# Performance work log

Hardware: AMD Instinct MI355X
Metric: run time of the kernel (lower is better)

Reference implementation:

```python
import jax, jax.numpy as jnp
import numpy as np

B, Hn, Wn, C, NH, WS, SR = 4, 64, 64, 256, 8, 3, 8
HD = C // NH
N = Hn * Wn
L = WS * WS
PH, PW = Hn // SR, Wn // SR
P = PH * PW
T = 4096  # cpb table length
NEG = -1e30

def _l2norm(x, axis=-1):
    return x / jnp.maximum(jnp.linalg.norm(x, axis=axis, keepdims=True), 1e-12)

def _unfold(x, ws):
    # x: (B, C, H, W) -> (B, C, ws*ws, H*W), torch F.unfold channel ordering (C major)
    p = ws // 2
    b, c, h, w = x.shape
    xp = jnp.pad(x, ((0, 0), (0, 0), (p, p), (p, p)))
    pats = jnp.stack([xp[:, :, i:i + h, j:j + w] for i in range(ws) for j in range(ws)], axis=2)
    return pats.reshape(b, c, ws * ws, h * w)

def setup_inputs():
    key = jax.random.key(0)
    ks = jax.random.split(key, 16)
    def w(k, shape, s=0.02):
        return jax.random.normal(k, shape, jnp.float32) * s
    # buffers derived from the window geometry (get_seqlen_and_mask)
    ones = np.ones((Hn, Wn), np.float32)
    pad = WS // 2
    op = np.pad(ones, pad)
    pats = np.stack([op[i:i + Hn, j:j + Wn] for i in range(WS) for j in range(WS)], -1).reshape(N, L)
    padding_mask = jnp.asarray(pats == 0)
    seq_length_scale = jnp.asarray(np.log(pats.sum(-1, keepdims=True) + P).astype(np.float32))
    temperature = jnp.log(jnp.expm1(jnp.ones((NH, 1, 1), jnp.float32) / 0.24))
    return dict(
        x=jax.random.normal(ks[0], (B, N, C), jnp.float32),
        relative_pos_index=jax.random.randint(ks[1], (N, P), 0, T),
        relative_coords_table=jax.random.uniform(ks[2], (T, 2), jnp.float32, -1.0, 1.0),
        q_w=w(ks[3], (C, C)), q_b=jnp.zeros((C,), jnp.float32),
        kv_w=w(ks[4], (2 * C, C)), kv_b=jnp.zeros((2 * C,), jnp.float32),
        temperature=temperature,
        query_embedding=w(ks[5], (NH, 1, HD)),
        proj_w=w(ks[6], (C, C)), proj_b=jnp.zeros((C,), jnp.float32),
        sr_w=w(ks[7], (C, C)), sr_b=jnp.zeros((C,), jnp.float32),
        norm_g=jnp.ones((C,), jnp.float32), norm_b=jnp.zeros((C,), jnp.float32),
        cpb1_w=w(ks[8], (512, 2)), cpb1_b=jnp.zeros((512,), jnp.float32),
        cpb2_w=w(ks[9], (NH, 512)), cpb2_b=jnp.zeros((NH,), jnp.float32),
        rpb_local=w(ks[10], (NH, L), 0.0004),
        learnable_tokens=w(ks[11], (NH, HD, L)),
        learnable_bias=jnp.zeros((NH, 1, L), jnp.float32),
        seq_length_scale=seq_length_scale,
        padding_mask=padding_mask,
        H=Hn, W=Wn,
    )

def _forward(x, q_w, q_b, kv_w, kv_b, temperature, query_embedding, proj_w, proj_b,
             sr_w, sr_b, norm_g, norm_b, cpb1_w, cpb1_b, cpb2_w, cpb2_b, rpb_local,
             learnable_tokens, learnable_bias, seq_length_scale, relative_coords_table,
             relative_pos_index, padding_mask, H, W):
    b, n, c = x.shape
    # normalized queries, scaled by learnable temperature and log-seqlen
    q = (x @ q_w.T + q_b).reshape(b, n, NH, HD).transpose(0, 2, 1, 3)  # (B,h,N,d)
    q_norm = _l2norm(q)
    q_scaled = (q_norm + query_embedding[None]) * jax.nn.softplus(temperature)[None] * seq_length_scale
    # --- local branch: sliding-window QK with RPB ---
    kv = x @ kv_w.T + kv_b  # (B,N,2C)
    k_loc = _l2norm((kv[..., :c]).reshape(b, n, NH, HD)).reshape(b, n, c)
    kv_img = jnp.concatenate([k_loc, kv[..., c:]], -1).transpose(0, 2, 1).reshape(b, 2 * c, H, W)
    pats = _unfold(kv_img, WS).reshape(b, 2 * NH, HD, L, n).transpose(0, 1, 4, 2, 3)  # (B,2h,N,d,L)
    k_loc, v_loc = pats[:, :NH], pats[:, NH:]
    attn_local = jnp.einsum('bhnd,bhndl->bhnl', q_scaled, k_loc) + rpb_local[None, :, None, :]
    attn_local = jnp.where(padding_mask[None, None], NEG, attn_local)
    # --- pooled branch ---
    x_img = x.transpose(0, 2, 1).reshape(b, c, H, W)
    x_sr = jax.nn.gelu(jnp.einsum('bchw,oc->bohw', x_img, sr_w) + sr_b[None, :, None, None], approximate=False)
    x_pool = x_sr.reshape(b, c, PH, SR, PW, SR).mean((3, 5)).reshape(b, c, P).transpose(0, 2, 1)  # (B,P,C)
    mu = x_pool.mean(-1, keepdims=True)
    var = x_pool.var(-1, keepdims=True)
    x_pool = (x_pool - mu) / jnp.sqrt(var + 1e-5) * norm_g + norm_b
    kv_pool = (x_pool @ kv_w.T + kv_b).reshape(b, P, 2 * NH, HD).transpose(0, 2, 1, 3)
    k_pool, v_pool = kv_pool[:, :NH], kv_pool[:, NH:]  # (B,h,P,d)
    cpb = jax.nn.relu(relative_coords_table @ cpb1_w.T + cpb1_b) @ cpb2_w.T + cpb2_b  # (T,h)
    pool_bias = cpb.T[:, relative_pos_index.reshape(-1)].reshape(NH, n, P)
    attn_pool = jnp.einsum('bhnd,bhpd->bhnp', q_scaled, _l2norm(k_pool)) + pool_bias[None]
    # --- joint softmax over local + pooled keys ---
    attn = jax.nn.softmax(jnp.concatenate([attn_local, attn_pool], -1), axis=-1)
    attn_local, attn_pool = attn[..., :L], attn[..., L:]
    a = jnp.einsum('bhnd,hdl->bhnl', q_norm, learnable_tokens) + learnable_bias[None] + attn_local
    x_local = jnp.einsum('bhnl,bhndl->bhnd', a, v_loc)
    x_pool_out = jnp.einsum('bhnp,bhpd->bhnd', attn_pool, v_pool)
    out = (x_local + x_pool_out).transpose(0, 2, 1, 3).reshape(b, n, c)
    return out @ proj_w.T + proj_b

def reference(x, relative_pos_index, relative_coords_table, q_w, q_b, kv_w, kv_b, temperature,
              query_embedding, proj_w, proj_b, sr_w, sr_b, norm_g, norm_b, cpb1_w, cpb1_b,
              cpb2_w, cpb2_b, rpb_local, learnable_tokens, learnable_bias, seq_length_scale,
              padding_mask, H, W):
    return _forward(x, q_w, q_b, kv_w, kv_b, temperature, query_embedding, proj_w, proj_b,
                    sr_w, sr_b, norm_g, norm_b, cpb1_w, cpb1_b, cpb2_w, cpb2_b, rpb_local,
                    learnable_tokens, learnable_bias, seq_length_scale, relative_coords_table,
                    relative_pos_index, padding_mask, H, W)
```

## Files before the change

### kernel.cpp

```cpp
#include <hip/hip_runtime.h>
#include <hip/hip_bf16.h>

typedef unsigned short u16;
typedef unsigned int u32;

#define B_ 4
#define N_ 4096
#define C_ 256
#define NH_ 8
#define HD_ 32
#define L_ 9
#define P_ 64
#define T_ 4096
#define NEG_ (-1e30f)

typedef __attribute__((ext_vector_type(8))) short bf16x8;
typedef __attribute__((ext_vector_type(4))) float f32x4;

__device__ __forceinline__ float b2f(u16 u) {
    union { u32 i; float f; } v; v.i = ((u32)u) << 16; return v.f;
}
__device__ __forceinline__ u16 f2b(float f) {
    u32 x = __float_as_uint(f);
    u32 r = (x + 0x7fffu + ((x >> 16) & 1u)) >> 16;
    return (u16)r;
}
__device__ __forceinline__ short f2bs(float f) { return (short)f2b(f); }

__global__ __launch_bounds__(256) void prep_k(
    const float* __restrict__ x, const float* __restrict__ q_w, const float* __restrict__ kv_w,
    const float* __restrict__ sr_w, const float* __restrict__ proj_w,
    u16* __restrict__ xb, u16* __restrict__ wfused, u16* __restrict__ pwb,
    const float* __restrict__ table, const float* __restrict__ w1, const float* __restrict__ b1,
    const float* __restrict__ w2, const float* __restrict__ b2, float* __restrict__ cpb)
{
    __shared__ float w1s[512][2];
    __shared__ float b1s[512];
    __shared__ float w2s[8][512];
    int bid = blockIdx.x, tid = threadIdx.x;
    if (bid < 4096) {
        int i = bid * 256 + tid;
        float4 v = reinterpret_cast<const float4*>(x)[i];
        ushort4 o; o.x = f2b(v.x); o.y = f2b(v.y); o.z = f2b(v.z); o.w = f2b(v.w);
        reinterpret_cast<ushort4*>(xb)[i] = o;
    } else if (bid < 4416) {
        int i = (bid - 4096) * 256 + tid;
        const float* s; u16* d; int off;
        if (i < 16384)      { s = q_w;    d = wfused; off = i; }
        else if (i < 49152) { s = kv_w;   d = wfused; off = i; }
        else if (i < 65536) { s = sr_w;   d = wfused; off = i; }
        else                { s = proj_w; d = pwb;    off = i - 65536; }
        int soff = (i < 16384) ? i : (i < 49152) ? (i - 16384) : (i < 65536) ? (i - 49152) : (i - 65536);
        float4 v = reinterpret_cast<const float4*>(s)[soff];
        ushort4 o; o.x = f2b(v.x); o.y = f2b(v.y); o.z = f2b(v.z); o.w = f2b(v.w);
        reinterpret_cast<ushort4*>(d)[off] = o;
    } else {
        for (int i = tid; i < 512; i += 256) {
            w1s[i][0] = w1[i * 2]; w1s[i][1] = w1[i * 2 + 1]; b1s[i] = b1[i];
        }
        for (int i = tid; i < 4096; i += 256) w2s[i >> 9][i & 511] = w2[i];
        __syncthreads();
        int t = (bid - 4416) * 256 + tid;
        float t0 = table[t * 2], t1 = table[t * 2 + 1];
        float acc[8] = {};
        for (int j = 0; j < 512; ++j) {
            float h = fmaxf(t0 * w1s[j][0] + t1 * w1s[j][1] + b1s[j], 0.0f);
            #pragma unroll
            for (int hh = 0; hh < 8; ++hh) acc[hh] += h * w2s[hh][j];
        }
        #pragma unroll
        for (int hh = 0; hh < 8; ++hh) cpb[t * 8 + hh] = acc[hh] + b2[hh];
    }
}

template<int MODE>
__global__ __launch_bounds__(256) void gemm_big_k(
    const u16* __restrict__ A, const u16* __restrict__ W,
    const float* __restrict__ b0, const float* __restrict__ b1, const float* __restrict__ b2,
    float* __restrict__ qn, float* __restrict__ kv, u16* __restrict__ xgb, float* __restrict__ pout)
{
    constexpr int RI = (MODE == 0) ? 4 : 1;
    __shared__ u16 Bs[64 * 264];
    int tid = threadIdx.x, w = tid >> 6, lane = tid & 63;
    int quad = lane >> 4, l16 = lane & 15;
    int colBase = blockIdx.x * 64;
    #pragma unroll
    for (int c = 0; c < 8; ++c) {
        int linear = c * 256 + tid;
        int col = linear >> 5, kc = linear & 31;
        uint4 v = *reinterpret_cast<const uint4*>(W + (size_t)(colBase + col) * 256 + kc * 8);
        *reinterpret_cast<uint4*>(&Bs[col * 264 + kc * 8]) = v;
    }
    __syncthreads();
    int rowBase = blockIdx.y * (RI * 64) + w * (RI * 16);
    f32x4 acc[RI][4] = {};
    const u16* aptr = A + (size_t)(rowBase + l16) * 256 + quad * 8;
    #pragma unroll
    for (int k0 = 0; k0 < 256; k0 += 32) {
        bf16x8 af[RI];
        #pragma unroll
        for (int i = 0; i < RI; ++i)
            af[i] = *reinterpret_cast<const bf16x8*>(aptr + (size_t)i * 16 * 256 + k0);
        #pragma unroll
        for (int j = 0; j < 4; ++j) {
            bf16x8 bfr = *reinterpret_cast<const bf16x8*>(&Bs[(j * 16 + l16) * 264 + k0 + quad * 8]);
            #pragma unroll
            for (int i = 0; i < RI; ++i)
                acc[i][j] = __builtin_amdgcn_mfma_f32_16x16x32_bf16(af[i], bfr, acc[i][j], 0, 0, 0);
        }
    }
    int rng = (MODE == 0) ? (colBase >> 8) : 99;
    float bj[4];
    #pragma unroll
    for (int j = 0; j < 4; ++j) {
        int gc = colBase + j * 16 + l16;
        if (MODE == 1)      bj[j] = b0[gc];
        else if (rng == 0)  bj[j] = b0[gc];
        else if (rng <= 2)  bj[j] = b1[gc - 256];
        else                bj[j] = b2[gc - 768];
    }
    #pragma unroll
    for (int i = 0; i < RI; ++i) {
        float vals[4][4];
        #pragma unroll
        for (int j = 0; j < 4; ++j)
            #pragma unroll
            for (int r = 0; r < 4; ++r) {
                float t = acc[i][j][r] + bj[j];
                if (MODE == 0 && rng == 3) t = 0.5f * t * (1.0f + erff(t * 0.70710678118654752f));
                vals[j][r] = t;
            }
        if (MODE == 0 && rng <= 1) {
            #pragma unroll
            for (int hp = 0; hp < 2; ++hp)
                #pragma unroll
                for (int r = 0; r < 4; ++r) {
                    float s = vals[2*hp][r] * vals[2*hp][r] + vals[2*hp+1][r] * vals[2*hp+1][r];
                    s += __shfl_xor(s, 1); s += __shfl_xor(s, 2);
                    s += __shfl_xor(s, 4); s += __shfl_xor(s, 8);
                    float inv = 1.0f / fmaxf(sqrtf(s), 1e-12f);
                    vals[2*hp][r] *= inv; vals[2*hp+1][r] *= inv;
                }
        }
        #pragma unroll
        for (int j = 0; j < 4; ++j) {
            int gc = colBase + j * 16 + l16;
            #pragma unroll
            for (int r = 0; r < 4; ++r) {
                int row = rowBase + i * 16 + quad * 4 + r;
                if (MODE == 1)      pout[(size_t)row * 256 + gc] = vals[j][r];
                else if (rng == 0)  qn[(size_t)row * 256 + gc] = vals[j][r];
                else if (rng <= 2)  kv[(size_t)row * 512 + gc - 256] = vals[j][r];
                else                xgb[(size_t)row * 256 + gc - 768] = f2b(vals[j][r]);
            }
        }
    }
}

__global__ __launch_bounds__(256) void poolkv_k(
    const u16* __restrict__ xgb, const float* __restrict__ g, const float* __restrict__ bta,
    const float* __restrict__ kv_w, const float* __restrict__ kv_b, float* __restrict__ kvp)
{
    __shared__ __align__(16) float xps[256];
    __shared__ float r1[4], r2[4];
    int bid = blockIdx.x;
    int bp = bid >> 1, half = bid & 1;
    int b = bp >> 6, p = bp & 63;
    int py = p >> 3, px = p & 7;
    int o = threadIdx.x;
    float s = 0.0f;
    for (int sy = 0; sy < 8; ++sy)
        #pragma unroll
        for (int sx = 0; sx < 8; ++sx) {
            int pix = (py * 8 + sy) * 64 + px * 8 + sx;
            s += b2f(xgb[((size_t)(b * N_ + pix)) * C_ + o]);
        }
    float v = s * (1.0f / 64.0f);
    float s1 = v, s2 = v * v;
    #pragma unroll
    for (int off = 32; off >= 1; off >>= 1) { s1 += __shfl_xor(s1, off); s2 += __shfl_xor(s2, off); }
    int wv = o >> 6, ln = o & 63;
    if (ln == 0) { r1[wv] = s1; r2[wv] = s2; }
    __syncthreads();
    float S1 = r1[0] + r1[1] + r1[2] + r1[3];
    float S2 = r2[0] + r2[1] + r2[2] + r2[3];
    float mu = S1 * (1.0f / 256.0f);
    float var = S2 * (1.0f / 256.0f) - mu * mu;
    xps[o] = (v - mu) * rsqrtf(var + 1e-5f) * g[o] + bta[o];
    __syncthreads();
    int col = half * 256 + o;
    float a = kv_b[col];
    const float4* xp4 = (const float4*)xps;
    const float4* wrow = (const float4*)(kv_w + (size_t)col * 256);
    #pragma unroll 8
    for (int k4 = 0; k4 < 64; ++k4) {
        float4 xv = xp4[k4]; float4 wa = wrow[k4];
        a += xv.x * wa.x + xv.y * wa.y + xv.z * wa.z + xv.w * wa.w;
    }
    if (half == 0) {
        float ss = a * a;
        ss += __shfl_xor(ss, 1); ss += __shfl_xor(ss, 2); ss += __shfl_xor(ss, 4);
        ss += __shfl_xor(ss, 8); ss += __shfl_xor(ss, 16);
        a *= 1.0f / fmaxf(sqrtf(ss), 1e-12f);
    }
    kvp[(size_t)bp * 512 + col] = a;
}

__global__ __launch_bounds__(256) void attn_k(
    const float* __restrict__ qn, const float* __restrict__ kv,
    const float* __restrict__ kvp, const float* __restrict__ cpb,
    const int* __restrict__ rpi, const float* __restrict__ temp,
    const float* __restrict__ qe, const float* __restrict__ lt,
    const float* __restrict__ rpb, const float* __restrict__ lb,
    const float* __restrict__ slsin, u16* __restrict__ aob)
{
    __shared__ u16 kp_hi[64 * 40], kp_lo[64 * 40];
    __shared__ u16 vp_hi[32 * 72], vp_lo[32 * 72];
    __shared__ u16 ltb[16 * 32];
    __shared__ float qs_w[4][16][36];
    __shared__ float S_w[4][16][76];
    __shared__ float aw_s[4][16][12];
    __shared__ float rpb_s[9], lb_s[9];

    int bid = blockIdx.x;
    int tile = bid & 63, h = (bid >> 6) & 7, b = bid >> 9;
    int tid = threadIdx.x, wave = tid >> 6, lane = tid & 63;
    int quad = lane >> 4, l16 = lane & 15;

    {
        int p = tid >> 2, dc = (tid & 3) * 8;
        const float* src = kvp + ((size_t)(b * P_ + p)) * 512 + h * 32 + dc;
        float4 k0 = *(const float4*)(src), k1 = *(const float4*)(src + 4);
        float4 v0 = *(const float4*)(src + 256), v1 = *(const float4*)(src + 260);
        float kf[8] = {k0.x,k0.y,k0.z,k0.w,k1.x,k1.y,k1.z,k1.w};
        float vf[8] = {v0.x,v0.y,v0.z,v0.w,v1.x,v1.y,v1.z,v1.w};
        #pragma unroll
        for (int j = 0; j < 8; ++j) {
            u16 khi = f2b(kf[j]);
            kp_hi[p * 40 + dc + j] = khi;
            kp_lo[p * 40 + dc + j] = f2b(kf[j] - b2f(khi));
            u16 vhi = f2b(vf[j]);
            vp_hi[(dc + j) * 72 + p] = vhi;
            vp_lo[(dc + j) * 72 + p] = f2b(vf[j] - b2f(vhi));
        }
    }
    for (int t = tid; t < 512; t += 256) {
        int l = t & 15, d = t >> 4;
        ltb[l * 32 + d] = (l < 9) ? f2b(lt[h * 288 + d * 9 + l]) : (u16)0;
    }
    if (tid < 9) { rpb_s[tid] = rpb[h * 9 + tid]; lb_s[tid] = lb[h * 9 + tid]; }
    float tsc = log1pf(expf(temp[h]));
    __syncthreads();

    int n0w = tile * 64 + wave * 16;
    bf16x8 qs_hi, qs_lo, qn_b;
    {
        int n = n0w + l16;
        const float* qptr = qn + ((size_t)(b * N_ + n)) * C_ + h * 32 + quad * 8;
        float4 q0 = *(const float4*)qptr, q1 = *(const float4*)(qptr + 4);
        const float* qeptr = qe + h * 32 + quad * 8;
        float4 e0 = *(const float4*)qeptr, e1 = *(const float4*)(qeptr + 4);
        float slv = slsin[n];
        float qf[8] = {q0.x,q0.y,q0.z,q0.w,q1.x,q1.y,q1.z,q1.w};
        float ef[8] = {e0.x,e0.y,e0.z,e0.w,e1.x,e1.y,e1.z,e1.w};
        #pragma unroll
        for (int j = 0; j < 8; ++j) {
            float qs = (qf[j] + ef[j]) * tsc * slv;
            u16 hi = f2b(qs);
            qs_hi[j] = (short)hi;
            qs_lo[j] = f2bs(qs - b2f(hi));
            qn_b[j]  = f2bs(qf[j]);
            qs_w[wave][l16][quad * 8 + j] = qs;
        }
        if (quad == 0) { S_w[wave][l16][73] = NEG_; S_w[wave][l16][74] = NEG_; S_w[wave][l16][75] = NEG_; }
    }

    #pragma unroll
    for (int jt = 0; jt < 4; ++jt) {
        bf16x8 bh = *(const bf16x8*)&kp_hi[(jt * 16 + l16) * 40 + quad * 8];
        bf16x8 bl = *(const bf16x8*)&kp_lo[(jt * 16 + l16) * 40 + quad * 8];
        f32x4 a = {};
        a = __builtin_amdgcn_mfma_f32_16x16x32_bf16(qs_lo, bh, a, 0, 0, 0);
        a = __builtin_amdgcn_mfma_f32_16x16x32_bf16(qs_hi, bl, a, 0, 0, 0);
        a = __builtin_amdgcn_mfma_f32_16x16x32_bf16(qs_hi, bh, a, 0, 0, 0);
        #pragma unroll
        for (int r = 0; r < 4; ++r) {
            int pix = quad * 4 + r;
            int n = n0w + pix;
            int idx = rpi[n * P_ + jt * 16 + l16];
            S_w[wave][pix][jt * 16 + l16] = a[r] + cpb[(size_t)idx * 8 + h];
        }
    }
    f32x4 accL;
    {
        bf16x8 ltf = *(const bf16x8*)&ltb[l16 * 32 + quad * 8];
        f32x4 z = {};
        accL = __builtin_amdgcn_mfma_f32_16x16x32_bf16(qn_b, ltf, z, 0, 0, 0);
    }
    for (int t = lane; t < 144; t += 64) {
        int pix = t / 9, l = t - pix * 9;
        int n = n0w + pix, y = n >> 6, x = n & 63;
        int ny = y + l / 3 - 1, nx = x + (l % 3) - 1;
        bool ok = ((unsigned)ny < 64u) && ((unsigned)nx < 64u);
        int nn = ok ? ny * 64 + nx : n;
        const float4* kb = (const float4*)(kv + ((size_t)(b * N_ + nn)) * 512 + h * 32);
        float acl = 0.0f;
        #pragma unroll
        for (int d4 = 0; d4 < 8; ++d4) {
            float4 kk = kb[d4];
            float4 qq = *(const float4*)&qs_w[wave][pix][d4 * 4];
            acl += qq.x * kk.x + qq.y * kk.y + qq.z * kk.z + qq.w * kk.w;
        }
        S_w[wave][pix][64 + l] = ok ? (acl + rpb_s[l]) : NEG_;
    }
    {
        int pix = lane >> 2, c0 = (lane & 3) * 19;
        float vals[19]; float mx = NEG_;
        #pragma unroll
        for (int i = 0; i < 19; ++i) { vals[i] = S_w[wave][pix][c0 + i]; mx = fmaxf(mx, vals[i]); }
        mx = fmaxf(mx, __shfl_xor(mx, 1));
        mx = fmaxf(mx, __shfl_xor(mx, 2));
        float sm = 0.0f;
        #pragma unroll
        for (int i = 0; i < 19; ++i) { vals[i] = expf(vals[i] - mx); sm += vals[i]; }
        sm += __shfl_xor(sm, 1); sm += __shfl_xor(sm, 2);
        float inv = 1.0f / sm;
        #pragma unroll
        for (int i = 0; i < 19; ++i) S_w[wave][pix][c0 + i] = vals[i] * inv;
    }
    if (l16 < 9) {
        #pragma unroll
        for (int r = 0; r < 4; ++r) {
            int pix = quad * 4 + r;
            int n = n0w + pix, y = n >> 6, x = n & 63;
            int ny = y + l16 / 3 - 1, nx = x + (l16 % 3) - 1;
            bool ok = ((unsigned)ny < 64u) && ((unsigned)nx < 64u);
            aw_s[wave][pix][l16] = ok ? (accL[r] + lb_s[l16] + S_w[wave][pix][64 + l16]) : 0.0f;
        }
    }
    f32x4 accO[2] = {};
    #pragma unroll
    for (int kc = 0; kc < 2; ++kc) {
        float wf[8];
        *(float4*)&wf[0] = *(const float4*)&S_w[wave][l16][kc * 32 + quad * 8];
        *(float4*)&wf[4] = *(const float4*)&S_w[wave][l16][kc * 32 + quad * 8 + 4];
        bf16x8 w_hi, w_lo;
        #pragma unroll
        for (int j = 0; j < 8; ++j) {
            u16 hi = f2b(wf[j]);
            w_hi[j] = (short)hi;
            w_lo[j] = f2bs(wf[j] - b2f(hi));
        }
        #pragma unroll
        for (int nt = 0; nt < 2; ++nt) {
            bf16x8 vh = *(const bf16x8*)&vp_hi[(nt * 16 + l16) * 72 + kc * 32 + quad * 8];
            bf16x8 vl = *(const bf16x8*)&vp_lo[(nt * 16 + l16) * 72 + kc * 32 + quad * 8];
            accO[nt] = __builtin_amdgcn_mfma_f32_16x16x32_bf16(w_lo, vh, accO[nt], 0, 0, 0);
            accO[nt] = __builtin_amdgcn_mfma_f32_16x16x32_bf16(w_hi, vl, accO[nt], 0, 0, 0);
            accO[nt] = __builtin_amdgcn_mfma_f32_16x16x32_bf16(w_hi, vh, accO[nt], 0, 0, 0);
        }
    }
    #pragma unroll
    for (int r = 0; r < 4; ++r) {
        int pix = quad * 4 + r;
        int n = n0w + pix, y = n >> 6, x = n & 63;
        #pragma unroll
        for (int l = 0; l < 9; ++l) {
            int ny = y + l / 3 - 1, nx = x + (l % 3) - 1;
            bool ok = ((unsigned)ny < 64u) && ((unsigned)nx < 64u);
            int nn = ok ? ny * 64 + nx : n;
            float aw = aw_s[wave][pix][l];
            const float* vb = kv + ((size_t)(b * N_ + nn)) * 512 + 256 + h * 32;
            accO[0][r] += aw * vb[l16];
            accO[1][r] += aw * vb[16 + l16];
        }
    }
    #pragma unroll
    for (int nt = 0; nt < 2; ++nt)
        #pragma unroll
        for (int r = 0; r < 4; ++r) {
            int n = n0w + quad * 4 + r;
            aob[((size_t)(b * N_ + n)) * C_ + h * 32 + nt * 16 + l16] = f2b(accO[nt][r]);
        }
}

extern "C" void kernel_launch(void* const* d_in, const int* in_sizes, int n_in,
                              void* d_out, int out_size, void* d_ws, size_t ws_size,
                              hipStream_t stream) {
    const float* x      = (const float*)d_in[0];
    const int*   rpi    = (const int*)d_in[1];
    const float* table  = (const float*)d_in[2];
    const float* q_w    = (const float*)d_in[3];
    const float* q_b    = (const float*)d_in[4];
    const float* kv_w   = (const float*)d_in[5];
    const float* kv_b   = (const float*)d_in[6];
    const float* temp   = (const float*)d_in[7];
    const float* qe     = (const float*)d_in[8];
    const float* proj_w = (const float*)d_in[9];
    const float* proj_b = (const float*)d_in[10];
    const float* sr_w   = (const float*)d_in[11];
    const float* sr_b   = (const float*)d_in[12];
    const float* norm_g = (const float*)d_in[13];
    const float* norm_b = (const float*)d_in[14];
    const float* cpb1_w = (const float*)d_in[15];
    const float* cpb1_b = (const float*)d_in[16];
    const float* cpb2_w = (const float*)d_in[17];
    const float* cpb2_b = (const float*)d_in[18];
    const float* rpb    = (const float*)d_in[19];
    const float* lt     = (const float*)d_in[20];
    const float* lb     = (const float*)d_in[21];
    const float* sls    = (const float*)d_in[22];

    float* ws  = (float*)d_ws;
    float* qn  = ws;
    float* kv  = qn  + (size_t)B_ * N_ * C_;
    float* kvp = kv  + (size_t)B_ * N_ * 2 * C_;
    float* cpb = kvp + (size_t)B_ * P_ * 2 * C_;
    u16*   xb  = (u16*)(cpb + (size_t)T_ * NH_);
    u16*   wfb = xb  + (size_t)B_ * N_ * C_;
    u16*   pwb = wfb + (size_t)1024 * C_;
    u16*   xgb = pwb + (size_t)C_ * C_;
    u16*   aob = xgb;

    dim3 blk(256);

    prep_k<<<dim3(4432), blk, 0, stream>>>(x, q_w, kv_w, sr_w, proj_w, xb, wfb, pwb,
                                           table, cpb1_w, cpb1_b, cpb2_w, cpb2_b, cpb);
    gemm_big_k<0><<<dim3(16, 64), blk, 0, stream>>>(xb, wfb, q_b, kv_b, sr_b, qn, kv, xgb, nullptr);
    poolkv_k<<<dim3(B_ * P_ * 2), blk, 0, stream>>>(xgb, norm_g, norm_b, kv_w, kv_b, kvp);
    attn_k<<<dim3(B_ * NH_ * 64), blk, 0, stream>>>(qn, kv, kvp, cpb, rpi, temp, qe, lt, rpb, lb, sls, aob);
    gemm_big_k<1><<<dim3(4, 256), blk, 0, stream>>>(aob, pwb, proj_b, nullptr, nullptr,
                                                    nullptr, nullptr, nullptr, (float*)d_out);
}
```

Baseline: 277.4 us.

## Prefetch GEMM A fragments and compute local QK dot products via lane shuffles

The GEMM kernel now double-buffers the A-operand register fragments, loading the next k-slice before issuing the MFMAs for the current one, so global-load latency overlaps compute. In the attention kernel the local-window Q·K dot products keep the scaled query in registers, split each dot product across the four quads and combine with xor shuffles, instead of staging the query in shared memory. The qs_w and aw_s shared buffers are removed, and the local attention weights are written back in place into S_w. This cuts LDS usage, which may allow more resident blocks, at the cost of extra live registers and shuffles.

```diff
diff --git a/kernel.cpp b/kernel.cpp
--- a/kernel.cpp
+++ b/kernel.cpp
@@ -95,18 +95,27 @@
     int rowBase = blockIdx.y * (RI * 64) + w * (RI * 16);
     f32x4 acc[RI][4] = {};
     const u16* aptr = A + (size_t)(rowBase + l16) * 256 + quad * 8;
+    bf16x8 afc[RI];
+    #pragma unroll
+    for (int i = 0; i < RI; ++i) afc[i] = *reinterpret_cast<const bf16x8*>(aptr + (size_t)i * 16 * 256);
     #pragma unroll
     for (int k0 = 0; k0 < 256; k0 += 32) {
-        bf16x8 af[RI];
-        #pragma unroll
-        for (int i = 0; i < RI; ++i)
-            af[i] = *reinterpret_cast<const bf16x8*>(aptr + (size_t)i * 16 * 256 + k0);
+        bf16x8 afn[RI];
+        if (k0 < 224) {
+            #pragma unroll
+            for (int i = 0; i < RI; ++i)
+                afn[i] = *reinterpret_cast<const bf16x8*>(aptr + (size_t)i * 16 * 256 + k0 + 32);
+        }
         #pragma unroll
         for (int j = 0; j < 4; ++j) {
             bf16x8 bfr = *reinterpret_cast<const bf16x8*>(&Bs[(j * 16 + l16) * 264 + k0 + quad * 8]);
             #pragma unroll
             for (int i = 0; i < RI; ++i)
-                acc[i][j] = __builtin_amdgcn_mfma_f32_16x16x32_bf16(af[i], bfr, acc[i][j], 0, 0, 0);
+                acc[i][j] = __builtin_amdgcn_mfma_f32_16x16x32_bf16(afc[i], bfr, acc[i][j], 0, 0, 0);
+        }
+        if (k0 < 224) {
+            #pragma unroll
+            for (int i = 0; i < RI; ++i) afc[i] = afn[i];
         }
     }
     int rng = (MODE == 0) ? (colBase >> 8) : 99;
@@ -217,9 +226,7 @@
     __shared__ u16 kp_hi[64 * 40], kp_lo[64 * 40];
     __shared__ u16 vp_hi[32 * 72], vp_lo[32 * 72];
     __shared__ u16 ltb[16 * 32];
-    __shared__ float qs_w[4][16][36];
     __shared__ float S_w[4][16][76];
-    __shared__ float aw_s[4][16][12];
     __shared__ float rpb_s[9], lb_s[9];
 
     int bid = blockIdx.x;
@@ -254,6 +261,7 @@
 
     int n0w = tile * 64 + wave * 16;
     bf16x8 qs_hi, qs_lo, qn_b;
+    float qsr[8];
     {
         int n = n0w + l16;
         const float* qptr = qn + ((size_t)(b * N_ + n)) * C_ + h * 32 + quad * 8;
@@ -270,7 +278,7 @@
             qs_hi[j] = (short)hi;
             qs_lo[j] = f2bs(qs - b2f(hi));
             qn_b[j]  = f2bs(qf[j]);
-            qs_w[wave][l16][quad * 8 + j] = qs;
+            qsr[j] = qs;
         }
         if (quad == 0) { S_w[wave][l16][73] = NEG_; S_w[wave][l16][74] = NEG_; S_w[wave][l16][75] = NEG_; }
     }
@@ -297,21 +305,19 @@
         f32x4 z = {};
         accL = __builtin_amdgcn_mfma_f32_16x16x32_bf16(qn_b, ltf, z, 0, 0, 0);
     }
-    for (int t = lane; t < 144; t += 64) {
-        int pix = t / 9, l = t - pix * 9;
-        int n = n0w + pix, y = n >> 6, x = n & 63;
+    #pragma unroll
+    for (int l = 0; l < 9; ++l) {
+        int n = n0w + l16, y = n >> 6, x = n & 63;
         int ny = y + l / 3 - 1, nx = x + (l % 3) - 1;
         bool ok = ((unsigned)ny < 64u) && ((unsigned)nx < 64u);
         int nn = ok ? ny * 64 + nx : n;
-        const float4* kb = (const float4*)(kv + ((size_t)(b * N_ + nn)) * 512 + h * 32);
-        float acl = 0.0f;
-        #pragma unroll
-        for (int d4 = 0; d4 < 8; ++d4) {
-            float4 kk = kb[d4];
-            float4 qq = *(const float4*)&qs_w[wave][pix][d4 * 4];
-            acl += qq.x * kk.x + qq.y * kk.y + qq.z * kk.z + qq.w * kk.w;
-        }
-        S_w[wave][pix][64 + l] = ok ? (acl + rpb_s[l]) : NEG_;
+        const float4* kb = (const float4*)(kv + ((size_t)(b * N_ + nn)) * 512 + h * 32 + quad * 8);
+        float4 k0v = kb[0], k1v = kb[1];
+        float part = qsr[0]*k0v.x + qsr[1]*k0v.y + qsr[2]*k0v.z + qsr[3]*k0v.w
+                   + qsr[4]*k1v.x + qsr[5]*k1v.y + qsr[6]*k1v.z + qsr[7]*k1v.w;
+        part += __shfl_xor(part, 16);
+        part += __shfl_xor(part, 32);
+        if (quad == 0) S_w[wave][l16][64 + l] = ok ? (part + rpb_s[l]) : NEG_;
     }
     {
         int pix = lane >> 2, c0 = (lane & 3) * 19;
@@ -335,7 +341,8 @@
             int n = n0w + pix, y = n >> 6, x = n & 63;
             int ny = y + l16 / 3 - 1, nx = x + (l16 % 3) - 1;
             bool ok = ((unsigned)ny < 64u) && ((unsigned)nx < 64u);
-            aw_s[wave][pix][l16] = ok ? (accL[r] + lb_s[l16] + S_w[wave][pix][64 + l16]) : 0.0f;
+            float prev = S_w[wave][pix][64 + l16];
+            S_w[wave][pix][64 + l16] = ok ? (accL[r] + lb_s[l16] + prev) : 0.0f;
         }
     }
     f32x4 accO[2] = {};
@@ -369,7 +376,7 @@
             int ny = y + l / 3 - 1, nx = x + (l % 3) - 1;
             bool ok = ((unsigned)ny < 64u) && ((unsigned)nx < 64u);
             int nn = ok ? ny * 64 + nx : n;
-            float aw = aw_s[wave][pix][l];
+            float aw = S_w[wave][pix][64 + l];
             const float* vb = kv + ((size_t)(b * N_ + nn)) * 512 + 256 + h * 32;
             accO[0][r] += aw * vb[l16];
             accO[1][r] += aw * vb[16 + l16];
```

Result: no change. 274.5 us (-1.1%).
